# Performance work log

Hardware: AMD Instinct MI355X
Metric: run time of the kernel (lower is better)

The kernel has to match this reference:

```python
import jax, jax.numpy as jnp
import numpy as np

HEADS = 8
DIM_HEAD = 64
SCALE = DIM_HEAD ** -0.5


def setup_inputs() -> dict:
    key = jax.random.key(0)
    k1, k2, k3 = jax.random.split(key, 3)
    B, N, D = 2, 2048, 1024
    dim_inner = HEADS * DIM_HEAD  # 512
    x = jax.random.normal(k1, (B, N, D), dtype=jnp.float32)
    W_qkv = jax.random.normal(k2, (6 * dim_inner, D), dtype=jnp.float32) * 0.02
    W_out = jax.random.normal(k3, (D, dim_inner), dtype=jnp.float32) * 0.02
    return {"x": x, "W_qkv": W_qkv, "W_out": W_out}


def reference(x, W_qkv, W_out):
    B, N, D = x.shape
    h, d = HEADS, DIM_HEAD

    # projection + split heads: 'b n (qkv h d) -> qkv b h n d'
    qkvs = x @ W_qkv.T                               # [B, N, 6*h*d]
    qkvs = qkvs.reshape(B, N, 6, h, d)
    qkvs = jnp.transpose(qkvs, (2, 0, 3, 1, 4))      # [6, B, h, N, d]
    qu, ku, vu, qc, kc, vc = qkvs

    qu_s = qu * SCALE
    qc_s = qc * SCALE

    neg = -jnp.finfo(x.dtype).max
    causal_mask = jnp.triu(jnp.ones((N, N), dtype=bool), 1)  # True strictly above diag

    # term1: qc . vu, zeroed strictly above diagonal
    term1 = jnp.einsum('bhid,bhjd->bhij', qc_s, vu)
    term1 = jnp.where(causal_mask, 0.0, term1)

    # lookahead attention: sigmoid(qu . ku), keep only strictly-upper part
    lookahead = jax.nn.sigmoid(jnp.einsum('bhid,bhjd->bhij', qu_s, ku))
    lookahead = jnp.where(causal_mask, lookahead, 0.0)

    Su = jnp.einsum('bhij,bhkj->bhik', term1, lookahead)
    Sc = jnp.einsum('bhid,bhjd->bhij', qc_s, kc)

    scores = Sc - jax.nn.silu(Su)
    scores = jnp.where(causal_mask, neg, scores)
    attn = jax.nn.softmax(scores, axis=-1)

    out = jnp.einsum('bhij,bhjd->bhid', attn, vc)    # [B, h, N, d]
    out = jnp.transpose(out, (0, 2, 1, 3)).reshape(B, N, h * d)
    return out @ W_out.T                             # [B, N, D]
```

## Files before the change

kernel.cpp:

```cpp
#include <hip/hip_runtime.h>
#include <cmath>

typedef unsigned short ushort_t;
typedef __attribute__((ext_vector_type(8))) short short8;
typedef __attribute__((ext_vector_type(4))) float f32x4;
typedef __attribute__((ext_vector_type(4))) short short4v;

static constexpr int NSEQ = 2048, DM = 1024, DI = 512;
static constexpr size_t NN = (size_t)NSEQ * NSEQ;

__device__ __forceinline__ ushort_t f2b(float v) {
    unsigned u = __float_as_uint(v);
    return (ushort_t)((u + 0x7fffu + ((u >> 16) & 1u)) >> 16);
}
__device__ __forceinline__ float b2f(ushort_t b) { return __uint_as_float(((unsigned)b) << 16); }
__device__ __forceinline__ float sigm(float x) { return 1.f / (1.f + expf(-x)); }
__device__ __forceinline__ float silu(float x) { return x / (1.f + expf(-x)); }

#define MFMA16(a, b, c) __builtin_amdgcn_mfma_f32_16x16x32_bf16(a, b, c, 0, 0, 0)

__device__ __forceinline__ void wait_vm8() { asm volatile("s_waitcnt vmcnt(8)" ::: "memory"); }
__device__ __forceinline__ void wait_vm3() { asm volatile("s_waitcnt vmcnt(3)" ::: "memory"); }
__device__ __forceinline__ void wait_vm4() { asm volatile("s_waitcnt vmcnt(4)" ::: "memory"); }
__device__ __forceinline__ void wait_vm0() { asm volatile("s_waitcnt vmcnt(0)" ::: "memory"); }

__device__ __forceinline__ void gll16(const ushort_t* g, ushort_t* l) {
    __builtin_amdgcn_global_load_lds((const __attribute__((address_space(1))) void*)g,
                                     (__attribute__((address_space(3))) void*)l, 16, 0, 0);
}
__device__ __forceinline__ void stage16(const ushort_t* g, int ldg, ushort_t* lds, int q) {
    const int l = threadIdx.x & 63;
    const int row = l >> 2;
    const int ch = (l & 3) ^ ((l >> 3) & 3);
    gll16(g + (size_t)(q * 16 + row) * ldg + ch * 8, lds + q * 512);
}
__device__ __forceinline__ short8 lfrag(const ushort_t* t, int row0, int lane) {
    const int row = row0 + (lane & 15);
    const int ch = (lane >> 4) ^ ((row >> 1) & 3);
    return *(const short8*)(t + row * 32 + (ch << 3));
}
__device__ __forceinline__ void mm32(const ushort_t* buf, int mb, int nb, int lane,
                                     f32x4 (&acc)[4][4]) {
    short8 fah[4], fal[4], fbh[4];
#pragma unroll
    for (int i = 0; i < 4; ++i) {
        fah[i] = lfrag(buf, mb + i * 16, lane);
        fal[i] = lfrag(buf + 4096, mb + i * 16, lane);
    }
#pragma unroll
    for (int j = 0; j < 4; ++j) fbh[j] = lfrag(buf + 8192, nb + j * 16, lane);
#pragma unroll
    for (int i = 0; i < 4; ++i)
#pragma unroll
        for (int j = 0; j < 4; ++j) {
            acc[i][j] = MFMA16(fah[i], fbh[j], acc[i][j]);
            acc[i][j] = MFMA16(fal[i], fbh[j], acc[i][j]);
        }
}
__device__ __forceinline__ void mm16(const ushort_t* buf, int mb, int nb, int lane,
                                     f32x4 (&acc)[4][4]) {
    short8 fah[4], fbh[4];
#pragma unroll
    for (int i = 0; i < 4; ++i) fah[i] = lfrag(buf, mb + i * 16, lane);
#pragma unroll
    for (int j = 0; j < 4; ++j) fbh[j] = lfrag(buf + 8192, nb + j * 16, lane);
#pragma unroll
    for (int i = 0; i < 4; ++i)
#pragma unroll
        for (int j = 0; j < 4; ++j) acc[i][j] = MFMA16(fah[i], fbh[j], acc[i][j]);
}
__device__ __forceinline__ void pair_decode(int p, int& lo, int& d) {
    d = 15;
    int cnt = 1;
    while (p >= cnt) { p -= cnt; --d; cnt = 16 - d; }
    lo = p;
}

__global__ __launch_bounds__(256) void k_cvt(const float4* __restrict__ src,
                                             ushort_t* __restrict__ hi,
                                             ushort_t* __restrict__ lo, int n4, int has_lo) {
    for (int i = blockIdx.x * 256 + threadIdx.x; i < n4; i += gridDim.x * 256) {
        float4 f = src[i];
        float a[4] = {f.x, f.y, f.z, f.w};
        short4v hv, lv;
#pragma unroll
        for (int j = 0; j < 4; ++j) {
            ushort_t h = f2b(a[j]);
            hv[j] = (short)h;
            lv[j] = (short)f2b(a[j] - b2f(h));
        }
        *(short4v*)(hi + (size_t)i * 4) = hv;
        if (has_lo) *(short4v*)(lo + (size_t)i * 4) = lv;
    }
}

__global__ __launch_bounds__(256) void k_proj(const ushort_t* __restrict__ xh,
                                              const ushort_t* __restrict__ xl,
                                              const ushort_t* __restrict__ wh,
                                              ushort_t* __restrict__ qh,
                                              ushort_t* __restrict__ vcT) {
    __shared__ __align__(16) ushort_t lds[2][12288];
    const int flat = blockIdx.x + 24 * blockIdx.y;
    const int p = (flat & 7) * 96 + (flat >> 3);
    const int bx = p % 24, by = p / 24;
    const int m0 = by * 128, n0 = bx * 128;
    const bool vconly = ((bx >> 2) == 5);
    const int l = threadIdx.x & 63, w = threadIdx.x >> 6;
    const int mb = (w >> 1) * 64, nb = (w & 1) * 64;
    const ushort_t* mats[3] = {xh + (size_t)m0 * DM, xl + (size_t)m0 * DM,
                               wh + (size_t)n0 * DM};
    const bool active = (w == 0) || (w == 2) || (w == 1 && !vconly);
    auto STAGE = [&](int t, ushort_t* buf) {
        if (!active) return;
        const ushort_t* src = mats[w] + t * 32;
        for (int q = 0; q < 8; ++q) stage16(src, DM, buf + w * 4096, q);
    };
    STAGE(0, lds[0]);
    f32x4 acc[4][4] = {};
    for (int t = 0; t < 32; ++t) {
        if (t + 1 < 32) {
            STAGE(t + 1, lds[(t + 1) & 1]);
            if (active) wait_vm8(); else wait_vm0();
        } else wait_vm0();
        __builtin_amdgcn_s_barrier();
        const ushort_t* buf = lds[t & 1];
        if (vconly) mm16(buf, mb, nb, l, acc);
        else mm32(buf, mb, nb, l, acc);
        __builtin_amdgcn_s_barrier();
    }
#pragma unroll
    for (int i = 0; i < 4; ++i)
#pragma unroll
        for (int j = 0; j < 4; ++j)
#pragma unroll
            for (int r = 0; r < 4; ++r) {
                int m = m0 + mb + i * 16 + (l >> 4) * 4 + r;
                int n = n0 + nb + j * 16 + (l & 15);
                float v = acc[i][j][r];
                int tt = n >> 9, head = (n >> 6) & 7, dd = n & 63;
                int b = m >> 11, np = m & 2047;
                if (tt == 0 || tt == 3) v *= 0.125f;
                ushort_t h = f2b(v);
                size_t off = (size_t)(tt * 16 + b * 8 + head) * 131072 + (size_t)np * 64 + dd;
                qh[off] = h;
                if (tt == 5) vcT[(size_t)(b * 8 + head) * 131072 + (size_t)dd * 2048 + np] = h;
            }
}

__global__ __launch_bounds__(256) void k_tl(const ushort_t* __restrict__ qkvh,
                                            ushort_t* __restrict__ Ph,
                                            ushort_t* __restrict__ t1dh,
                                            ushort_t* __restrict__ lkdh, int g0) {
    const int mode = blockIdx.x & 1, z = blockIdx.x >> 1, hh = g0 + z;
    int lo_t, d;
    pair_decode(blockIdx.y, lo_t, d);
    const int by = mode ? lo_t : lo_t + d;
    const int bx = mode ? lo_t + d : lo_t;
    __shared__ __align__(16) ushort_t lds[2][8192];
    const int l = threadIdx.x & 63, w = threadIdx.x >> 6;
    const int mb = (w >> 1) * 64, nb = (w & 1) * 64;
    const int ta = mode ? 0 : 3, tb = mode ? 1 : 2;
    const ushort_t* matA = qkvh + (size_t)(ta * 16 + hh) * 131072 + (size_t)(by * 128) * 64;
    const ushort_t* matB = qkvh + (size_t)(tb * 16 + hh) * 131072 + (size_t)(bx * 128) * 64;
    auto STAGE = [&](int t, ushort_t* buf) {
        if (w == 0) for (int q = 0; q < 8; ++q) stage16(matA + t * 32, 64, buf, q);
        else if (w == 1) for (int q = 0; q < 8; ++q) stage16(matB + t * 32, 64, buf + 4096, q);
    };
    STAGE(0, lds[0]);
    __syncthreads();
    f32x4 acc[4][4] = {};
    for (int t = 0; t < 2; ++t) {
        if (t == 0) STAGE(1, lds[1]);
        const ushort_t* buf = lds[t & 1];
        short8 fah[4], fbh[4];
#pragma unroll
        for (int i = 0; i < 4; ++i) fah[i] = lfrag(buf, mb + i * 16, l);
#pragma unroll
        for (int j = 0; j < 4; ++j) fbh[j] = lfrag(buf + 4096, nb + j * 16, l);
#pragma unroll
        for (int i = 0; i < 4; ++i)
#pragma unroll
            for (int j = 0; j < 4; ++j) acc[i][j] = MFMA16(fah[i], fbh[j], acc[i][j]);
        __syncthreads();
    }
    const bool isdiag = (bx == by);
    ushort_t* ph = Ph + (size_t)z * NN;
    if (mode == 0) {
        ushort_t* dh = t1dh + ((size_t)z * 16 + by) * 16384;
#pragma unroll
        for (int i = 0; i < 4; ++i)
#pragma unroll
            for (int j = 0; j < 4; ++j)
#pragma unroll
                for (int r = 0; r < 4; ++r) {
                    int gi = by * 128 + mb + i * 16 + (l >> 4) * 4 + r;
                    int gj = bx * 128 + nb + j * 16 + (l & 15);
                    ushort_t h = f2b(acc[i][j][r]);
                    if (gj <= gi) ph[(size_t)gi * 2048 + gj] = h;
                    if (isdiag) dh[(gi & 127) * 128 + (gj & 127)] = (gj <= gi) ? h : 0;
                }
    } else {
        ushort_t* dh = lkdh + ((size_t)z * 16 + by) * 16384;
#pragma unroll
        for (int i = 0; i < 4; ++i)
#pragma unroll
            for (int j = 0; j < 4; ++j)
#pragma unroll
                for (int r = 0; r < 4; ++r) {
                    int gk = by * 128 + mb + i * 16 + (l >> 4) * 4 + r;
                    int gj = bx * 128 + nb + j * 16 + (l & 15);
                    ushort_t h = f2b(sigm(acc[i][j][r]));
                    if (gj > gk) ph[(size_t)gk * 2048 + gj] = h;
                    if (isdiag) dh[(gk & 127) * 128 + (gj & 127)] = (gj > gk) ? h : 0;
                }
    }
}

__global__ __launch_bounds__(256) void k_scores(const ushort_t* __restrict__ Ph,
                                                const ushort_t* __restrict__ t1dh,
                                                const ushort_t* __restrict__ lkdh,
                                                const ushort_t* __restrict__ qkvh,
                                                float* __restrict__ sc, int g0) {
    const int z = blockIdx.x, hh = g0 + z;
    int bxk, d;
    pair_decode(blockIdx.y, bxk, d);
    const int byi = bxk + d;
    __shared__ __align__(16) ushort_t lds[3][8192];
    const int l = threadIdx.x & 63, w = threadIdx.x >> 6;
    const int mb = (w >> 1) * 64, nb = (w & 1) * 64;
    const int nsu = (d + 1) * 4, nt = nsu + 2;
    const ushort_t* pAh = Ph + (size_t)z * NN + (size_t)(byi * 128) * 2048;
    const ushort_t* pBh = Ph + (size_t)z * NN + (size_t)(bxk * 128) * 2048;
    const ushort_t* dAh = t1dh + ((size_t)z * 16 + byi) * 16384;
    const ushort_t* dBh = lkdh + ((size_t)z * 16 + bxk) * 16384;
    const ushort_t* qch = qkvh + (size_t)(3 * 16 + hh) * 131072 + (size_t)(byi * 128) * 64;
    const ushort_t* kch = qkvh + (size_t)(4 * 16 + hh) * 131072 + (size_t)(bxk * 128) * 64;
    const bool stager = (w == 0 || w == 2);
    auto STAGE = [&](int t, ushort_t* buf) {
        if (t >= nt || !stager) return;
        const ushort_t* src;
        int ld;
        if (t < nsu) {
            const int tb = t >> 2, kloc = (t & 3) * 32;
            if (w == 0) {
                if (tb == d) { src = dAh + kloc; ld = 128; }
                else { src = pAh + (bxk + tb) * 128 + kloc; ld = 2048; }
            } else {
                if (tb == 0) { src = dBh + kloc; ld = 128; }
                else { src = pBh + (bxk + tb) * 128 + kloc; ld = 2048; }
            }
        } else {
            const int k0 = (t - nsu) * 32;
            src = (w == 0) ? qch + k0 : kch + k0;
            ld = 64;
        }
        ushort_t* dst = buf + ((w == 0) ? 0 : 4096);
        for (int q = 0; q < 8; ++q) stage16(src, ld, dst, q);
    };
    STAGE(0, lds[0]);
    STAGE(1, lds[1]);
    f32x4 acc[4][4] = {};
    for (int t = 0; t < nt; ++t) {
        if (t + 1 < nt && stager) wait_vm8(); else wait_vm0();
        __builtin_amdgcn_s_barrier();
        STAGE(t + 2, lds[(t + 2) % 3]);
        if (t == nsu) {
#pragma unroll
            for (int i = 0; i < 4; ++i)
#pragma unroll
                for (int j = 0; j < 4; ++j)
#pragma unroll
                    for (int r = 0; r < 4; ++r) acc[i][j][r] = -silu(acc[i][j][r]);
        }
        const ushort_t* buf = lds[t % 3];
        short8 fah[4], fbh[4];
#pragma unroll
        for (int i = 0; i < 4; ++i) fah[i] = lfrag(buf, mb + i * 16, l);
#pragma unroll
        for (int j = 0; j < 4; ++j) fbh[j] = lfrag(buf + 4096, nb + j * 16, l);
#pragma unroll
        for (int i = 0; i < 4; ++i)
#pragma unroll
            for (int j = 0; j < 4; ++j) acc[i][j] = MFMA16(fah[i], fbh[j], acc[i][j]);
    }
    float* so = sc + (size_t)z * NN;
#pragma unroll
    for (int i = 0; i < 4; ++i)
#pragma unroll
        for (int j = 0; j < 4; ++j)
#pragma unroll
            for (int r = 0; r < 4; ++r) {
                int gi = byi * 128 + mb + i * 16 + (l >> 4) * 4 + r;
                int gk = bxk * 128 + nb + j * 16 + (l & 15);
                if (gk <= gi) so[(size_t)gi * 2048 + gk] = acc[i][j][r];
            }
}

__global__ __launch_bounds__(256) void k_softmax(const float* __restrict__ scb,
                                                 ushort_t* __restrict__ attn) {
    const int z = blockIdx.x >> 11, i = blockIdx.x & 2047;
    const float* scr = scb + (size_t)z * NN + (size_t)i * 2048;
    ushort_t* arow = attn + (size_t)z * NN + (size_t)i * 2048;
    const int tid = threadIdx.x, k0 = tid * 8;
    float sv[8];
    if (k0 <= i) {
        float4 a0 = *(const float4*)(scr + k0), a1 = *(const float4*)(scr + k0 + 4);
        sv[0] = a0.x; sv[1] = a0.y; sv[2] = a0.z; sv[3] = a0.w;
        sv[4] = a1.x; sv[5] = a1.y; sv[6] = a1.z; sv[7] = a1.w;
    } else {
#pragma unroll
        for (int e = 0; e < 8; ++e) sv[e] = -3e38f;
    }
    float s[8];
    float m = -3e38f;
#pragma unroll
    for (int e = 0; e < 8; ++e) {
        s[e] = (k0 + e <= i) ? sv[e] : -3e38f;
        m = fmaxf(m, s[e]);
    }
    __shared__ float red[256];
    red[tid] = m;
    __syncthreads();
    for (int ss = 128; ss; ss >>= 1) {
        if (tid < ss) red[tid] = fmaxf(red[tid], red[tid + ss]);
        __syncthreads();
    }
    m = red[0];
    __syncthreads();
    float p[8], sum = 0.f;
#pragma unroll
    for (int e = 0; e < 8; ++e) { p[e] = expf(s[e] - m); sum += p[e]; }
    red[tid] = sum;
    __syncthreads();
    for (int ss = 128; ss; ss >>= 1) {
        if (tid < ss) red[tid] += red[tid + ss];
        __syncthreads();
    }
    const float inv = 1.f / red[0];
    const int lim = ((i >> 7) + 1) << 7;
    if (k0 < lim) {
        short8 o;
#pragma unroll
        for (int e = 0; e < 8; ++e) o[e] = (short)f2b(p[e] * inv);
        *(short8*)(arow + k0) = o;
    }
}

__global__ __launch_bounds__(256) void k_pv(const ushort_t* __restrict__ attn,
                                            const ushort_t* __restrict__ vcT,
                                            float* __restrict__ opbase, int g0) {
    const int z = blockIdx.x, hh = g0 + z;
    int pp = blockIdx.y, byi = 15, c;
    for (;;) {
        int cb = (byi >> 2) + 1;
        if (pp < cb) { c = pp; break; }
        pp -= cb;
        --byi;
    }
    const int nt = min(4, byi + 1 - c * 4) * 4;
    const ushort_t* ap = attn + (size_t)z * NN + (size_t)(byi * 128) * 2048 + c * 512;
    const ushort_t* vp = vcT + (size_t)hh * 131072 + c * 512;
    float* op = opbase + (size_t)z * NN + (size_t)(c * 2048) * 64;
    __shared__ __align__(16) ushort_t lds[3][6144];
    const int l = threadIdx.x & 63, w = threadIdx.x >> 6, mb = w * 32;
    auto STAGE = [&](int t, ushort_t* buf) {
        const int k0 = t * 32;
        for (int u = w * 3; u < w * 3 + 3; ++u) {
            if (u < 8) stage16(ap + k0, 2048, buf, u);
            else stage16(vp + k0, 2048, buf + 4096, u - 8);
        }
    };
    STAGE(0, lds[0]);
    STAGE(1, lds[1]);
    f32x4 acc[2][4] = {};
    for (int t = 0; t < nt; ++t) {
        if (t + 1 < nt) wait_vm3(); else wait_vm0();
        __builtin_amdgcn_s_barrier();
        if (t + 2 < nt) STAGE(t + 2, lds[(t + 2) % 3]);
        const ushort_t* buf = lds[t % 3];
        short8 fa[2], fb[4];
#pragma unroll
        for (int i = 0; i < 2; ++i) fa[i] = lfrag(buf, mb + i * 16, l);
#pragma unroll
        for (int j = 0; j < 4; ++j) fb[j] = lfrag(buf + 4096, j * 16, l);
#pragma unroll
        for (int i = 0; i < 2; ++i)
#pragma unroll
            for (int j = 0; j < 4; ++j) acc[i][j] = MFMA16(fa[i], fb[j], acc[i][j]);
    }
#pragma unroll
    for (int i = 0; i < 2; ++i)
#pragma unroll
        for (int j = 0; j < 4; ++j)
#pragma unroll
            for (int r = 0; r < 4; ++r) {
                int gi = byi * 128 + mb + i * 16 + (l >> 4) * 4 + r;
                int dd = j * 16 + (l & 15);
                op[(size_t)gi * 64 + dd] = acc[i][j][r];
            }
}

__global__ __launch_bounds__(256) void k_pvc(const float* __restrict__ opall,
                                             ushort_t* __restrict__ attno, int g0) {
    const int z = blockIdx.x >> 9, rem = blockIdx.x & 511;
    const int i = rem * 4 + (threadIdx.x >> 6), d = threadIdx.x & 63;
    const int hh = g0 + z, b = hh >> 3, h = hh & 7;
    const float* op = opall + (size_t)z * NN;
    const int nc = (i >> 9) + 1;
    float a = 0.f;
    for (int c = 0; c < nc; ++c) a += op[(size_t)(c * 2048 + i) * 64 + d];
    attno[(size_t)(b * 2048 + i) * 512 + h * 64 + d] = f2b(a);
}

__global__ __launch_bounds__(256) void k_outproj(const ushort_t* __restrict__ attno,
                                                 const ushort_t* __restrict__ woh,
                                                 float* __restrict__ out) {
    __shared__ __align__(16) ushort_t lds[3][8192];
    const int m0 = blockIdx.y * 128, n0 = blockIdx.x * 128;
    const int l = threadIdx.x & 63, w = threadIdx.x >> 6;
    const int mb = (w >> 1) * 64, nb = (w & 1) * 64;
    const ushort_t* pa = attno + (size_t)m0 * DI;
    const ushort_t* pb = woh + (size_t)n0 * DI;
    auto STAGE = [&](int t, ushort_t* buf) {
        const int k0 = t * 32;
        for (int u = w * 4; u < w * 4 + 4; ++u) {
            if (u < 8) stage16(pa + k0, DI, buf, u);
            else stage16(pb + k0, DI, buf + 4096, u - 8);
        }
    };
    STAGE(0, lds[0]);
    STAGE(1, lds[1]);
    f32x4 acc[4][4] = {};
    for (int t = 0; t < 16; ++t) {
        if (t + 1 < 16) wait_vm4(); else wait_vm0();
        __builtin_amdgcn_s_barrier();
        if (t + 2 < 16) STAGE(t + 2, lds[(t + 2) % 3]);
        const ushort_t* buf = lds[t % 3];
        short8 fa[4], fb[4];
#pragma unroll
        for (int i = 0; i < 4; ++i) fa[i] = lfrag(buf, mb + i * 16, l);
#pragma unroll
        for (int j = 0; j < 4; ++j) fb[j] = lfrag(buf + 4096, nb + j * 16, l);
#pragma unroll
        for (int i = 0; i < 4; ++i)
#pragma unroll
            for (int j = 0; j < 4; ++j) acc[i][j] = MFMA16(fa[i], fb[j], acc[i][j]);
    }
#pragma unroll
    for (int i = 0; i < 4; ++i)
#pragma unroll
        for (int j = 0; j < 4; ++j)
#pragma unroll
            for (int r = 0; r < 4; ++r) {
                int m = m0 + mb + i * 16 + (l >> 4) * 4 + r;
                int n = n0 + nb + j * 16 + (l & 15);
                out[(size_t)m * DM + n] = acc[i][j][r];
            }
}

extern "C" void kernel_launch(void* const* d_in, const int* in_sizes, int n_in,
                              void* d_out, int out_size, void* d_ws, size_t ws_size,
                              hipStream_t stream) {
    const float* x = (const float*)d_in[0];
    const float* Wqkv = (const float*)d_in[1];
    const float* Wout = (const float*)d_in[2];
    float* out = (float*)d_out;

    const size_t fixedb = 33554432ull;
    const size_t perh = 26214400ull;
    int g = 0;
    for (int cand : {16, 8, 4, 2, 1})
        if (fixedb + perh * (size_t)cand <= ws_size) { g = cand; break; }
    if (!g) return;

    ushort_t* qh = (ushort_t*)d_ws;
    ushort_t* vcT = qh + 12582912;
    ushort_t* attno = vcT + 2097152;
    ushort_t* pool = attno + 2097152;
    ushort_t* xh = pool;
    ushort_t* xl = xh + 4194304;
    ushort_t* wh = xl + 4194304;
    ushort_t* Ph = pool;
    ushort_t* t1dh = Ph + (size_t)g * NN;
    ushort_t* lkdh = t1dh + (size_t)g * 262144;
    float* scf = (float*)(lkdh + (size_t)g * 262144);
    ushort_t* woh = pool;

    k_cvt<<<dim3(1024), 256, 0, stream>>>((const float4*)x, xh, xl, 1048576, 1);
    k_cvt<<<dim3(1024), 256, 0, stream>>>((const float4*)Wqkv, wh, nullptr, 786432, 0);
    k_proj<<<dim3(24, 32), 256, 0, stream>>>(xh, xl, wh, qh, vcT);

    for (int g0 = 0; g0 < 16; g0 += g) {
        k_tl<<<dim3(2 * g, 136), 256, 0, stream>>>(qh, Ph, t1dh, lkdh, g0);
        k_scores<<<dim3(g, 136), 256, 0, stream>>>(Ph, t1dh, lkdh, qh, scf, g0);
        k_softmax<<<dim3(2048 * g), 256, 0, stream>>>(scf, Ph);
        k_pv<<<dim3(g, 40), 256, 0, stream>>>(Ph, vcT, scf, g0);
        k_pvc<<<dim3(512 * g), 256, 0, stream>>>(scf, attno, g0);
    }

    k_cvt<<<dim3(512), 256, 0, stream>>>((const float4*)Wout, woh, nullptr, 131072, 0);
    k_outproj<<<dim3(8, 32), 256, 0, stream>>>(attno, woh, out);
}
```

Measured before the change: 373.6 us.

## Drop low-part split of x in QKV projection and triple-buffer LDS staging

Measured after the change: 349.1 us. 1.07x faster.

```diff
diff --git a/kernel.cpp b/kernel.cpp
--- a/kernel.cpp
+++ b/kernel.cpp
@@ -38,36 +38,6 @@
     const int row = row0 + (lane & 15);
     const int ch = (lane >> 4) ^ ((row >> 1) & 3);
     return *(const short8*)(t + row * 32 + (ch << 3));
-}
-__device__ __forceinline__ void mm32(const ushort_t* buf, int mb, int nb, int lane,
-                                     f32x4 (&acc)[4][4]) {
-    short8 fah[4], fal[4], fbh[4];
-#pragma unroll
-    for (int i = 0; i < 4; ++i) {
-        fah[i] = lfrag(buf, mb + i * 16, lane);
-        fal[i] = lfrag(buf + 4096, mb + i * 16, lane);
-    }
-#pragma unroll
-    for (int j = 0; j < 4; ++j) fbh[j] = lfrag(buf + 8192, nb + j * 16, lane);
-#pragma unroll
-    for (int i = 0; i < 4; ++i)
-#pragma unroll
-        for (int j = 0; j < 4; ++j) {
-            acc[i][j] = MFMA16(fah[i], fbh[j], acc[i][j]);
-            acc[i][j] = MFMA16(fal[i], fbh[j], acc[i][j]);
-        }
-}
-__device__ __forceinline__ void mm16(const ushort_t* buf, int mb, int nb, int lane,
-                                     f32x4 (&acc)[4][4]) {
-    short8 fah[4], fbh[4];
-#pragma unroll
-    for (int i = 0; i < 4; ++i) fah[i] = lfrag(buf, mb + i * 16, lane);
-#pragma unroll
-    for (int j = 0; j < 4; ++j) fbh[j] = lfrag(buf + 8192, nb + j * 16, lane);
-#pragma unroll
-    for (int i = 0; i < 4; ++i)
-#pragma unroll
-        for (int j = 0; j < 4; ++j) acc[i][j] = MFMA16(fah[i], fbh[j], acc[i][j]);
 }
 __device__ __forceinline__ void pair_decode(int p, int& lo, int& d) {
     d = 15;
@@ -95,38 +65,42 @@
 }
 
 __global__ __launch_bounds__(256) void k_proj(const ushort_t* __restrict__ xh,
-                                              const ushort_t* __restrict__ xl,
                                               const ushort_t* __restrict__ wh,
                                               ushort_t* __restrict__ qh,
                                               ushort_t* __restrict__ vcT) {
-    __shared__ __align__(16) ushort_t lds[2][12288];
+    __shared__ __align__(16) ushort_t lds[3][8192];
     const int flat = blockIdx.x + 24 * blockIdx.y;
     const int p = (flat & 7) * 96 + (flat >> 3);
     const int bx = p % 24, by = p / 24;
     const int m0 = by * 128, n0 = bx * 128;
-    const bool vconly = ((bx >> 2) == 5);
     const int l = threadIdx.x & 63, w = threadIdx.x >> 6;
     const int mb = (w >> 1) * 64, nb = (w & 1) * 64;
-    const ushort_t* mats[3] = {xh + (size_t)m0 * DM, xl + (size_t)m0 * DM,
-                               wh + (size_t)n0 * DM};
-    const bool active = (w == 0) || (w == 2) || (w == 1 && !vconly);
+    const ushort_t* matA = xh + (size_t)m0 * DM;
+    const ushort_t* matB = wh + (size_t)n0 * DM;
+    const bool stager = (w == 0 || w == 1);
     auto STAGE = [&](int t, ushort_t* buf) {
-        if (!active) return;
-        const ushort_t* src = mats[w] + t * 32;
-        for (int q = 0; q < 8; ++q) stage16(src, DM, buf + w * 4096, q);
+        if (t >= 32 || !stager) return;
+        const ushort_t* src = (w == 0) ? matA + t * 32 : matB + t * 32;
+        ushort_t* dst = buf + ((w == 0) ? 0 : 4096);
+        for (int q = 0; q < 8; ++q) stage16(src, DM, dst, q);
     };
     STAGE(0, lds[0]);
+    STAGE(1, lds[1]);
     f32x4 acc[4][4] = {};
     for (int t = 0; t < 32; ++t) {
-        if (t + 1 < 32) {
-            STAGE(t + 1, lds[(t + 1) & 1]);
-            if (active) wait_vm8(); else wait_vm0();
-        } else wait_vm0();
+        if (t + 1 < 32 && stager) wait_vm8(); else wait_vm0();
         __builtin_amdgcn_s_barrier();
-        const ushort_t* buf = lds[t & 1];
-        if (vconly) mm16(buf, mb, nb, l, acc);
-        else mm32(buf, mb, nb, l, acc);
-        __builtin_amdgcn_s_barrier();
+        STAGE(t + 2, lds[(t + 2) % 3]);
+        const ushort_t* buf = lds[t % 3];
+        short8 fah[4], fbh[4];
+#pragma unroll
+        for (int i = 0; i < 4; ++i) fah[i] = lfrag(buf, mb + i * 16, l);
+#pragma unroll
+        for (int j = 0; j < 4; ++j) fbh[j] = lfrag(buf + 4096, nb + j * 16, l);
+#pragma unroll
+        for (int i = 0; i < 4; ++i)
+#pragma unroll
+            for (int j = 0; j < 4; ++j) acc[i][j] = MFMA16(fah[i], fbh[j], acc[i][j]);
     }
 #pragma unroll
     for (int i = 0; i < 4; ++i)
@@ -478,17 +452,16 @@
     ushort_t* attno = vcT + 2097152;
     ushort_t* pool = attno + 2097152;
     ushort_t* xh = pool;
-    ushort_t* xl = xh + 4194304;
-    ushort_t* wh = xl + 4194304;
+    ushort_t* wh = xh + 4194304;
     ushort_t* Ph = pool;
     ushort_t* t1dh = Ph + (size_t)g * NN;
     ushort_t* lkdh = t1dh + (size_t)g * 262144;
     float* scf = (float*)(lkdh + (size_t)g * 262144);
     ushort_t* woh = pool;
 
-    k_cvt<<<dim3(1024), 256, 0, stream>>>((const float4*)x, xh, xl, 1048576, 1);
+    k_cvt<<<dim3(1024), 256, 0, stream>>>((const float4*)x, xh, nullptr, 1048576, 0);
     k_cvt<<<dim3(1024), 256, 0, stream>>>((const float4*)Wqkv, wh, nullptr, 786432, 0);
-    k_proj<<<dim3(24, 32), 256, 0, stream>>>(xh, xl, wh, qh, vcT);
+    k_proj<<<dim3(24, 32), 256, 0, stream>>>(xh, wh, qh, vcT);
 
     for (int g0 = 0; g0 < 16; g0 += g) {
         k_tl<<<dim3(2 * g, 136), 256, 0, stream>>>(qh, Ph, t1dh, lkdh, g0);
```
